# Performance work log

Hardware: AMD Instinct MI355X
Metric: run time of the kernel (lower is better)

Reference implementation:

```python
import jax, jax.numpy as jnp
import numpy as np

B, D, O = 16384, 1024, 2048
MU, LAM = 0.9, 0.1


def setup_inputs() -> dict:
    key = jax.random.key(0)
    ks = jax.random.split(key, 16)
    stdv = float(1.0 / np.sqrt(D))
    u = lambda k, shape, s: jax.random.uniform(k, shape, jnp.float32, -s, s)
    return {
        "x": jax.random.normal(ks[0], (B, D), jnp.float32),
        "x_ctx": jax.random.normal(ks[1], (B, D), jnp.float32),
        "classifier": u(ks[2], (O, D), stdv),
        "none_tensor": u(ks[3], (1, D), stdv),
        "ctx_q_w": u(ks[4], (O, D), stdv),
        "ctx_q_b": u(ks[5], (O,), stdv),
        "word_g_w": u(ks[6], (1, D), stdv),
        "word_g_b": u(ks[7], (1,), stdv),
        "tcq_w1": u(ks[8], (D, D), stdv),
        "tcq_b1": u(ks[9], (D,), stdv),
        "tcq_w2": u(ks[10], (O, D), stdv),
        "tcq_b2": u(ks[11], (O,), stdv),
        "history_input": 0.1 * jax.random.normal(ks[12], (O - 1, D), jnp.float32),
        "history_count": jax.random.randint(ks[13], (O - 1,), 0, 10),
        "labels": jax.random.randint(ks[14], (B,), 0, O),
    }


def reference(x, x_ctx, classifier, none_tensor, ctx_q_w, ctx_q_b,
              word_g_w, word_g_b, tcq_w1, tcq_b1, tcq_w2, tcq_b2,
              history_input, history_count, labels):
    mu, lam = MU, LAM
    # ---- update_history (torch.no_grad), vectorized over classes via segment_sum ----
    xs = jax.lax.stop_gradient(x)
    sums = jax.ops.segment_sum(xs, labels, num_segments=O)               # [O, D]
    counts = jax.ops.segment_sum(jnp.ones((B,), jnp.float32), labels, num_segments=O)  # [O]
    has = counts[1:] > 0                                                  # classes 1..O-1
    cls_mean = sums[1:] / jnp.maximum(counts[1:], 1.0)[:, None]
    hist = jnp.where(has[:, None], mu * history_input + cls_mean, history_input)
    cnt = history_count + has.astype(history_count.dtype)
    # ---- generate_substitute (mu < 1 branch) ----
    denom = 1.0 - jnp.power(mu, jnp.maximum(cnt, 1).astype(jnp.float32))[:, None]
    v = hist * (1.0 - mu) / denom                                        # [O-1, D]
    r_sub = jnp.concatenate([none_tensor, v], axis=0)                    # [O, D]
    ctx_logits = x_ctx @ ctx_q_w.T + ctx_q_b                              # [B, O]
    att_logits = jax.nn.gelu(x @ tcq_w1.T + tcq_b1, approximate=False) @ tcq_w2.T + tcq_b2  # [B, O]
    # ---- gated combine + bilinear classifier (training=True path: w uses ctx_logits) ----
    g_word = jax.nn.sigmoid(x @ word_g_w.T + word_g_b)                    # [B, 1]
    w = g_word * jax.nn.sigmoid(ctx_logits)                               # [B, O]
    # logits = sum(((1-w)*x[:,None,:] + w*r_sub) * classifier, -1), collapsed algebraically
    logits = (1.0 - w) * (x @ classifier.T) + w * jnp.einsum('od,od->o', r_sub, classifier)[None, :]
    # ---- losses on labels >= 0 (mask-weighted means, jit-safe) ----
    mask = (labels >= 0).astype(jnp.float32)
    n = jnp.maximum(mask.sum(), 1.0)
    lsm = jax.nn.log_softmax(logits, axis=-1)
    nll = -jnp.take_along_axis(lsm, jnp.maximum(labels, 0)[:, None], axis=1)[:, 0]
    ce = (mask * nll).sum() / n
    mse_row = jnp.mean((ctx_logits - att_logits) ** 2, axis=-1)
    mse = (mask * mse_row).sum() / n
    return (ce + lam * mse, logits)
```

## Files before the change

### kernel.cpp

```cpp
#include <hip/hip_runtime.h>
#include <cstdint>
#include <cstddef>

#define DEV __device__ __forceinline__

typedef __attribute__((ext_vector_type(4))) float f32x4;
typedef __attribute__((ext_vector_type(8))) short bf16x8;
typedef unsigned short ushort_t;
typedef __attribute__((ext_vector_type(8))) unsigned short ushort8;

static constexpr int B_ = 16384, D_ = 1024, O_ = 2048;
static constexpr float LAM_ = 0.1f;

static constexpr size_t WS_XBF   = 0;
static constexpr size_t WS_XCBF  = WS_XBF   + (size_t)B_ * D_ * 2;
static constexpr size_t WS_HBF   = WS_XCBF  + (size_t)B_ * D_ * 2;
static constexpr size_t WS_CLSBF = WS_HBF   + (size_t)B_ * D_ * 2;
static constexpr size_t WS_CTWBF = WS_CLSBF + (size_t)O_ * D_ * 2;
static constexpr size_t WS_W2BF  = WS_CTWBF + (size_t)O_ * D_ * 2;
static constexpr size_t WS_W1BF  = WS_W2BF  + (size_t)O_ * D_ * 2;
static constexpr size_t WS_SMALL = WS_W1BF  + (size_t)D_ * D_ * 2;
static constexpr size_t SM_COUNTS = 0;
static constexpr size_t SM_TSUM   = 8192;
static constexpr size_t SM_MSE    = 16384;
static constexpr size_t SM_ZERO_BYTES = 82176;
static constexpr size_t SM_S      = 82176;
static constexpr size_t SM_GWORD  = 90368;
static constexpr size_t SM_CEROW  = 155904;

DEV float wave_sum(float v) {
  #pragma unroll
  for (int o = 32; o; o >>= 1) v += __shfl_xor(v, o, 64);
  return v;
}

DEV ushort_t f2bf1(float f) {
  union { float f; unsigned u; } c{f};
  unsigned r = c.u + 0x7fffu + ((c.u >> 16) & 1u);
  return (ushort_t)(r >> 16);
}

DEV float sigmoidf(float z) { return 1.0f / (1.0f + expf(-z)); }

DEV void gload_lds16(const ushort_t* g, ushort_t* l) {
  __builtin_amdgcn_global_load_lds((const __attribute__((address_space(1))) void*)g,
                                   (__attribute__((address_space(3))) void*)l, 16, 0, 0);
}

DEV f32x4 mfma16(bf16x8 a, bf16x8 b, f32x4 c) {
  return __builtin_amdgcn_mfma_f32_16x16x32_bf16(a, b, c, 0, 0, 0);
}

#define DSR(dst, addr, off) \
  asm volatile("ds_read_b128 %0, %1 offset:" off : "=v"(dst) : "v"(addr))

__global__ __launch_bounds__(256) void f2bf_kernel(const float* __restrict__ in,
                                                   ushort_t* __restrict__ out, int n8) {
  int i = blockIdx.x * 256 + threadIdx.x;
  if (i >= n8) return;
  const float4* p = (const float4*)(in + (size_t)i * 8);
  float4 a = p[0], b = p[1];
  ushort8 o;
  o[0] = f2bf1(a.x); o[1] = f2bf1(a.y); o[2] = f2bf1(a.z); o[3] = f2bf1(a.w);
  o[4] = f2bf1(b.x); o[5] = f2bf1(b.y); o[6] = f2bf1(b.z); o[7] = f2bf1(b.w);
  *(ushort8*)(out + (size_t)i * 8) = o;
}

__global__ __launch_bounds__(256) void rowdot_kernel(const float* __restrict__ x,
    const float* __restrict__ cls, const float* __restrict__ wg,
    const float* __restrict__ wgb, const int* __restrict__ labels,
    float* __restrict__ tsum, float* __restrict__ counts, float* __restrict__ g_word) {
  int wave = threadIdx.x >> 6, lane = threadIdx.x & 63;
  int row = blockIdx.x * 4 + wave;
  const float* xr = x + (size_t)row * D_;
  int lab = labels[row];
  const float* cr = cls + (size_t)max(lab, 0) * D_;
  float t = 0.f, g = 0.f;
  #pragma unroll
  for (int j = 0; j < 4; ++j) {
    int d = j * 256 + lane * 4;
    float4 xv = *(const float4*)(xr + d);
    float4 cv = *(const float4*)(cr + d);
    float4 wv = *(const float4*)(wg + d);
    t += xv.x * cv.x + xv.y * cv.y + xv.z * cv.z + xv.w * cv.w;
    g += xv.x * wv.x + xv.y * wv.y + xv.z * wv.z + xv.w * wv.w;
  }
  t = wave_sum(t); g = wave_sum(g);
  if (lane == 0) {
    if (lab >= 0) {
      atomicAdd(&tsum[lab], t);
      atomicAdd(&counts[lab], 1.0f);
    }
    g_word[row] = sigmoidf(g + wgb[0]);
  }
}

__global__ __launch_bounds__(256) void scls_kernel(const float* __restrict__ cls,
    const float* __restrict__ none_t, const float* __restrict__ hist,
    const int* __restrict__ hcnt, const float* __restrict__ counts,
    const float* __restrict__ tsum, float* __restrict__ s) {
  int wave = threadIdx.x >> 6, lane = threadIdx.x & 63;
  int o = blockIdx.x * 4 + wave;
  if (o >= O_) return;
  const float* cr = cls + (size_t)o * D_;
  const float* src = (o == 0) ? none_t : hist + (size_t)(o - 1) * D_;
  float dv = 0.f;
  #pragma unroll
  for (int j = 0; j < 4; ++j) {
    int d = j * 256 + lane * 4;
    float4 a = *(const float4*)(src + d);
    float4 c = *(const float4*)(cr + d);
    dv += a.x * c.x + a.y * c.y + a.z * c.z + a.w * c.w;
  }
  dv = wave_sum(dv);
  if (lane == 0) {
    if (o == 0) { s[0] = dv; }
    else {
      float co = counts[o];
      bool has = co > 0.f;
      int cnt = hcnt[o - 1] + (has ? 1 : 0);
      float denom = 1.f - powf(0.9f, (float)max(cnt, 1));
      float val = has ? (0.9f * dv + tsum[o] / fmaxf(co, 1.f)) : dv;
      s[o] = (0.1f / denom) * val;
    }
  }
}

template<int EPI, int NBN>
__global__ __launch_bounds__(512, 4) void gemm8_kernel(
    const ushort_t* __restrict__ A, const ushort_t* __restrict__ Bmat,
    const float* __restrict__ bias, float* __restrict__ fout,
    ushort_t* __restrict__ hout, const float* __restrict__ g_word,
    const float* __restrict__ svec, float* __restrict__ mse_row) {
  __shared__ __align__(16) ushort_t lds[36864];
  const int tid = threadIdx.x, lane = tid & 63, wave = tid >> 6;
  const int wr = wave >> 1, wc = wave & 1;
  const int nwg = 64 * NBN, cpx = nwg >> 3;
  int bid = blockIdx.x;
  int wg = (bid & 7) * cpx + (bid >> 3);
  const int bm = wg / NBN, bn = wg % NBN;
  const int NCOL = NBN * 128;
  const int qsrc = (tid & 3) ^ ((tid >> 3) & 3);
  const ushort_t* sA0 = A + ((size_t)bm * 256 + (tid >> 2)) * 1024 + qsrc * 8;
  const ushort_t* sB0 = Bmat + ((size_t)bn * 128 + (tid >> 2)) * 1024 + qsrc * 8;
  const int qrd = (lane >> 4) ^ (((lane & 15) >> 1) & 3);
  const unsigned aoffB = (unsigned)(((wr * 64 + (lane & 15)) * 32 + qrd * 8) * 2);
  const unsigned boffB = (unsigned)(((wc * 64 + (lane & 15)) * 32 + qrd * 8) * 2) + 49152u;
  f32x4 acc[4][4] = {};
  gload_lds16(sA0, lds + tid * 8);
  gload_lds16(sA0 + 128 * 1024, lds + (tid + 512) * 8);
  gload_lds16(sB0, lds + 24576 + tid * 8);
  gload_lds16(sA0 + 32, lds + 8192 + tid * 8);
  gload_lds16(sA0 + 32 + 128 * 1024, lds + 8192 + (tid + 512) * 8);
  gload_lds16(sB0 + 32, lds + 24576 + 4096 + tid * 8);
  asm volatile("s_waitcnt vmcnt(3)" ::: "memory");
  __builtin_amdgcn_s_barrier();
  #pragma unroll
  for (int t = 0; t < 32; ++t) {
    const unsigned aA = aoffB + (unsigned)((t % 3) * 16384);
    const unsigned aB = boffB + (unsigned)((t % 3) * 8192);
    bf16x8 fA[4], fB[4];
    DSR(fB[0], aB, "0"); DSR(fB[1], aB, "1024");
    DSR(fB[2], aB, "2048"); DSR(fB[3], aB, "3072");
    DSR(fA[0], aA, "0"); DSR(fA[1], aA, "1024");
    DSR(fA[2], aA, "2048"); DSR(fA[3], aA, "3072");
    if (t < 30) {
      const ushort_t* srcA = sA0 + (size_t)(t + 2) * 32;
      const ushort_t* srcB = sB0 + (size_t)(t + 2) * 32;
      ushort_t* dA = lds + ((t + 2) % 3) * 8192;
      ushort_t* dB = lds + 24576 + ((t + 2) % 3) * 4096;
      gload_lds16(srcA, dA + tid * 8);
      gload_lds16(srcA + 128 * 1024, dA + (tid + 512) * 8);
      gload_lds16(srcB, dB + tid * 8);
    }
    __builtin_amdgcn_s_barrier();
    asm volatile("s_waitcnt lgkmcnt(0)");
    __builtin_amdgcn_sched_barrier(0);
    __builtin_amdgcn_s_setprio(1);
    #pragma unroll
    for (int m = 0; m < 4; m++)
      #pragma unroll
      for (int n = 0; n < 4; n++) acc[m][n] = mfma16(fA[m], fB[n], acc[m][n]);
    __builtin_amdgcn_s_setprio(0);
    __builtin_amdgcn_sched_barrier(0);
    if (t < 30)      asm volatile("s_waitcnt vmcnt(3)" ::: "memory");
    else if (t == 30) asm volatile("s_waitcnt vmcnt(0)" ::: "memory");
    __builtin_amdgcn_s_barrier();
  }
  #pragma unroll
  for (int m = 0; m < 4; m++) {
    #pragma unroll
    for (int i = 0; i < 4; i++) {
      int row = bm * 256 + wr * 64 + m * 16 + (lane >> 4) * 4 + i;
      float gw = 0.f, msum = 0.f;
      if constexpr (EPI == 3) gw = g_word[row];
      #pragma unroll
      for (int n = 0; n < 4; n++) {
        int col = bn * 128 + wc * 64 + n * 16 + (lane & 15);
        float v = acc[m][n][i];
        if constexpr (EPI == 0) {
          float z = v + bias[col];
          float gl = 0.5f * z * (1.f + erff(z * 0.70710678118f));
          hout[(size_t)row * 1024 + col] = f2bf1(gl);
        } else if constexpr (EPI == 1) {
          fout[(size_t)row * NCOL + col] = v + bias[col];
        } else if constexpr (EPI == 2) {
          float att = v + bias[col];
          float ctx = fout[(size_t)row * NCOL + col];
          float d = ctx - att;
          msum += d * d;
        } else {
          size_t off = (size_t)row * NCOL + col;
          float ctx = fout[off];
          float w = gw * sigmoidf(ctx);
          fout[off] = (1.f - w) * v + w * svec[col];
        }
      }
      if constexpr (EPI == 2) {
        #pragma unroll
        for (int o = 1; o < 16; o <<= 1) msum += __shfl_xor(msum, o, 64);
        if ((lane & 15) == 0) atomicAdd(&mse_row[row], msum);
      }
    }
  }
}

__global__ __launch_bounds__(256) void ce_kernel(const float* __restrict__ logits,
    const int* __restrict__ labels, float* __restrict__ ce_row) {
  int row = blockIdx.x, t = threadIdx.x, lane = t & 63, wave = t >> 6;
  const float* lr = logits + (size_t)row * O_;
  float v[8];
  float m = -INFINITY;
  #pragma unroll
  for (int j = 0; j < 8; j++) { v[j] = lr[t + j * 256]; m = fmaxf(m, v[j]); }
  #pragma unroll
  for (int o = 32; o; o >>= 1) m = fmaxf(m, __shfl_xor(m, o, 64));
  __shared__ float red[8];
  if (lane == 0) red[wave] = m;
  __syncthreads();
  m = fmaxf(fmaxf(red[0], red[1]), fmaxf(red[2], red[3]));
  float se = 0.f;
  #pragma unroll
  for (int j = 0; j < 8; j++) se += expf(v[j] - m);
  se = wave_sum(se);
  if (lane == 0) red[4 + wave] = se;
  __syncthreads();
  if (t == 0) {
    float bs = red[4] + red[5] + red[6] + red[7];
    int lab = labels[row];
    float nll = 0.f;
    if (lab >= 0) nll = -(lr[lab] - m - logf(bs));
    ce_row[row] = nll;
  }
}

__global__ __launch_bounds__(256) void finalize_kernel(const float* __restrict__ ce_row,
    const float* __restrict__ mse_row, const int* __restrict__ labels,
    float* __restrict__ out0) {
  int t = threadIdx.x, lane = t & 63, wave = t >> 6;
  float sn = 0.f, sm = 0.f, sc = 0.f;
  for (int i = t; i < B_; i += 256) {
    if (labels[i] >= 0) { sn += ce_row[i]; sm += mse_row[i]; sc += 1.f; }
  }
  sn = wave_sum(sn); sm = wave_sum(sm); sc = wave_sum(sc);
  __shared__ float r0[4], r1[4], r2[4];
  if (lane == 0) { r0[wave] = sn; r1[wave] = sm; r2[wave] = sc; }
  __syncthreads();
  if (t == 0) {
    float a = r0[0] + r0[1] + r0[2] + r0[3];
    float b = r1[0] + r1[1] + r1[2] + r1[3];
    float c = r2[0] + r2[1] + r2[2] + r2[3];
    out0[0] = (a + LAM_ * (b / (float)O_)) / fmaxf(c, 1.f);
  }
}

extern "C" void kernel_launch(void* const* d_in, const int* in_sizes, int n_in,
                              void* d_out, int out_size, void* d_ws, size_t ws_size,
                              hipStream_t stream) {
  const float* x        = (const float*)d_in[0];
  const float* x_ctx    = (const float*)d_in[1];
  const float* cls      = (const float*)d_in[2];
  const float* none_t   = (const float*)d_in[3];
  const float* ctx_q_w  = (const float*)d_in[4];
  const float* ctx_q_b  = (const float*)d_in[5];
  const float* word_g_w = (const float*)d_in[6];
  const float* word_g_b = (const float*)d_in[7];
  const float* w1       = (const float*)d_in[8];
  const float* b1       = (const float*)d_in[9];
  const float* w2       = (const float*)d_in[10];
  const float* b2       = (const float*)d_in[11];
  const float* hist     = (const float*)d_in[12];
  const int*   hcnt     = (const int*)d_in[13];
  const int*   labels   = (const int*)d_in[14];

  float* out  = (float*)d_out;
  float* out1 = out + 1;
  char* ws = (char*)d_ws;

  ushort_t* xbf   = (ushort_t*)(ws + WS_XBF);
  ushort_t* xcbf  = (ushort_t*)(ws + WS_XCBF);
  ushort_t* hbf   = (ushort_t*)(ws + WS_HBF);
  ushort_t* clsbf = (ushort_t*)(ws + WS_CLSBF);
  ushort_t* ctwbf = (ushort_t*)(ws + WS_CTWBF);
  ushort_t* w2bf  = (ushort_t*)(ws + WS_W2BF);
  ushort_t* w1bf  = (ushort_t*)(ws + WS_W1BF);
  float* counts   = (float*)(ws + WS_SMALL + SM_COUNTS);
  float* tsum     = (float*)(ws + WS_SMALL + SM_TSUM);
  float* mse_row  = (float*)(ws + WS_SMALL + SM_MSE);
  float* s        = (float*)(ws + WS_SMALL + SM_S);
  float* g_word   = (float*)(ws + WS_SMALL + SM_GWORD);
  float* ce_row   = (float*)(ws + WS_SMALL + SM_CEROW);

  hipMemsetAsync(ws + WS_SMALL, 0, SM_ZERO_BYTES, stream);

  f2bf_kernel<<<8192, 256, 0, stream>>>(x, xbf, B_ * D_ / 8);
  f2bf_kernel<<<8192, 256, 0, stream>>>(x_ctx, xcbf, B_ * D_ / 8);
  f2bf_kernel<<<1024, 256, 0, stream>>>(cls, clsbf, O_ * D_ / 8);
  f2bf_kernel<<<1024, 256, 0, stream>>>(ctx_q_w, ctwbf, O_ * D_ / 8);
  f2bf_kernel<<<1024, 256, 0, stream>>>(w2, w2bf, O_ * D_ / 8);
  f2bf_kernel<<<512, 256, 0, stream>>>(w1, w1bf, D_ * D_ / 8);

  rowdot_kernel<<<B_ / 4, 256, 0, stream>>>(x, cls, word_g_w, word_g_b, labels,
                                            tsum, counts, g_word);
  scls_kernel<<<O_ / 4, 256, 0, stream>>>(cls, none_t, hist, hcnt, counts, tsum, s);

  gemm8_kernel<0, 8><<<512, 512, 0, stream>>>(xbf, w1bf, b1, nullptr, hbf,
                                              nullptr, nullptr, nullptr);
  gemm8_kernel<1, 16><<<1024, 512, 0, stream>>>(xcbf, ctwbf, ctx_q_b, out1, nullptr,
                                                nullptr, nullptr, nullptr);
  gemm8_kernel<2, 16><<<1024, 512, 0, stream>>>(hbf, w2bf, b2, out1, nullptr,
                                                nullptr, nullptr, mse_row);
  gemm8_kernel<3, 16><<<1024, 512, 0, stream>>>(xbf, clsbf, nullptr, out1, nullptr,
                                                g_word, s, nullptr);

  ce_kernel<<<B_, 256, 0, stream>>>(out1, labels, ce_row);
  finalize_kernel<<<1, 256, 0, stream>>>(ce_row, mse_row, labels, out);
}
```

Baseline: 478.4 us.

## Replace pipelined 256x128 GEMM with simple 128x128 tiles and bf16 ctx buffer

New measurement: 456.1 us. 4.7% less time.

```diff
diff --git a/kernel.cpp b/kernel.cpp
--- a/kernel.cpp
+++ b/kernel.cpp
@@ -27,6 +27,8 @@
 static constexpr size_t SM_S      = 82176;
 static constexpr size_t SM_GWORD  = 90368;
 static constexpr size_t SM_CEROW  = 155904;
+static constexpr size_t WS_CTXBF  = WS_SMALL + 2 * 1024 * 1024;
+static constexpr size_t WS_NEED_BIG = WS_CTXBF + (size_t)B_ * O_ * 2;
 
 DEV float wave_sum(float v) {
   #pragma unroll
@@ -40,6 +42,11 @@
   return (ushort_t)(r >> 16);
 }
 
+DEV float bf2f(ushort_t u) {
+  union { unsigned u; float f; } c{(unsigned)u << 16};
+  return c.f;
+}
+
 DEV float sigmoidf(float z) { return 1.0f / (1.0f + expf(-z)); }
 
 DEV void gload_lds16(const ushort_t* g, ushort_t* l) {
@@ -47,12 +54,17 @@
                                    (__attribute__((address_space(3))) void*)l, 16, 0, 0);
 }
 
+DEV void stage128s(const ushort_t* __restrict__ src, ushort_t* lds_, int tid) {
+  int c0 = tid, c1 = tid + 256;
+  int q0 = (c0 & 3) ^ ((c0 >> 3) & 3);
+  int q1 = (c1 & 3) ^ ((c1 >> 3) & 3);
+  gload_lds16(src + (size_t)(c0 >> 2) * 1024 + q0 * 8, lds_ + c0 * 8);
+  gload_lds16(src + (size_t)(c1 >> 2) * 1024 + q1 * 8, lds_ + c1 * 8);
+}
+
 DEV f32x4 mfma16(bf16x8 a, bf16x8 b, f32x4 c) {
   return __builtin_amdgcn_mfma_f32_16x16x32_bf16(a, b, c, 0, 0, 0);
 }
-
-#define DSR(dst, addr, off) \
-  asm volatile("ds_read_b128 %0, %1 offset:" off : "=v"(dst) : "v"(addr))
 
 __global__ __launch_bounds__(256) void f2bf_kernel(const float* __restrict__ in,
                                                    ushort_t* __restrict__ out, int n8) {
@@ -66,9 +78,10 @@
   *(ushort8*)(out + (size_t)i * 8) = o;
 }
 
-__global__ __launch_bounds__(256) void rowdot_kernel(const float* __restrict__ x,
+__global__ __launch_bounds__(256) void rowdot_cvt_kernel(const float* __restrict__ x,
     const float* __restrict__ cls, const float* __restrict__ wg,
     const float* __restrict__ wgb, const int* __restrict__ labels,
+    ushort_t* __restrict__ xbf,
     float* __restrict__ tsum, float* __restrict__ counts, float* __restrict__ g_word) {
   int wave = threadIdx.x >> 6, lane = threadIdx.x & 63;
   int row = blockIdx.x * 4 + wave;
@@ -84,6 +97,10 @@
     float4 wv = *(const float4*)(wg + d);
     t += xv.x * cv.x + xv.y * cv.y + xv.z * cv.z + xv.w * cv.w;
     g += xv.x * wv.x + xv.y * wv.y + xv.z * wv.z + xv.w * wv.w;
+    uint2 pk;
+    pk.x = (unsigned)f2bf1(xv.x) | ((unsigned)f2bf1(xv.y) << 16);
+    pk.y = (unsigned)f2bf1(xv.z) | ((unsigned)f2bf1(xv.w) << 16);
+    *(uint2*)(xbf + (size_t)row * D_ + d) = pk;
   }
   t = wave_sum(t); g = wave_sum(g);
   if (lane == 0) {
@@ -126,72 +143,47 @@
   }
 }
 
-template<int EPI, int NBN>
-__global__ __launch_bounds__(512, 4) void gemm8_kernel(
+template<int EPI, int NBN, bool CTXB>
+__global__ __launch_bounds__(256, 3) void gemm128_kernel(
     const ushort_t* __restrict__ A, const ushort_t* __restrict__ Bmat,
     const float* __restrict__ bias, float* __restrict__ fout,
-    ushort_t* __restrict__ hout, const float* __restrict__ g_word,
-    const float* __restrict__ svec, float* __restrict__ mse_row) {
-  __shared__ __align__(16) ushort_t lds[36864];
+    ushort_t* __restrict__ hout, ushort_t* __restrict__ ctxbf,
+    const float* __restrict__ g_word, const float* __restrict__ svec,
+    float* __restrict__ mse_row) {
+  __shared__ __align__(16) ushort_t As[128 * 32], Bs[128 * 32];
   const int tid = threadIdx.x, lane = tid & 63, wave = tid >> 6;
   const int wr = wave >> 1, wc = wave & 1;
-  const int nwg = 64 * NBN, cpx = nwg >> 3;
   int bid = blockIdx.x;
-  int wg = (bid & 7) * cpx + (bid >> 3);
-  const int bm = wg / NBN, bn = wg % NBN;
+  int group = bid / (8 * NBN), within = bid % (8 * NBN);
+  int bm = group * 8 + (within & 7);
+  int bn = within >> 3;
   const int NCOL = NBN * 128;
-  const int qsrc = (tid & 3) ^ ((tid >> 3) & 3);
-  const ushort_t* sA0 = A + ((size_t)bm * 256 + (tid >> 2)) * 1024 + qsrc * 8;
-  const ushort_t* sB0 = Bmat + ((size_t)bn * 128 + (tid >> 2)) * 1024 + qsrc * 8;
-  const int qrd = (lane >> 4) ^ (((lane & 15) >> 1) & 3);
-  const unsigned aoffB = (unsigned)(((wr * 64 + (lane & 15)) * 32 + qrd * 8) * 2);
-  const unsigned boffB = (unsigned)(((wc * 64 + (lane & 15)) * 32 + qrd * 8) * 2) + 49152u;
   f32x4 acc[4][4] = {};
-  gload_lds16(sA0, lds + tid * 8);
-  gload_lds16(sA0 + 128 * 1024, lds + (tid + 512) * 8);
-  gload_lds16(sB0, lds + 24576 + tid * 8);
-  gload_lds16(sA0 + 32, lds + 8192 + tid * 8);
-  gload_lds16(sA0 + 32 + 128 * 1024, lds + 8192 + (tid + 512) * 8);
-  gload_lds16(sB0 + 32, lds + 24576 + 4096 + tid * 8);
-  asm volatile("s_waitcnt vmcnt(3)" ::: "memory");
-  __builtin_amdgcn_s_barrier();
-  #pragma unroll
-  for (int t = 0; t < 32; ++t) {
-    const unsigned aA = aoffB + (unsigned)((t % 3) * 16384);
-    const unsigned aB = boffB + (unsigned)((t % 3) * 8192);
-    bf16x8 fA[4], fB[4];
-    DSR(fB[0], aB, "0"); DSR(fB[1], aB, "1024");
-    DSR(fB[2], aB, "2048"); DSR(fB[3], aB, "3072");
-    DSR(fA[0], aA, "0"); DSR(fA[1], aA, "1024");
-    DSR(fA[2], aA, "2048"); DSR(fA[3], aA, "3072");
-    if (t < 30) {
-      const ushort_t* srcA = sA0 + (size_t)(t + 2) * 32;
-      const ushort_t* srcB = sB0 + (size_t)(t + 2) * 32;
-      ushort_t* dA = lds + ((t + 2) % 3) * 8192;
-      ushort_t* dB = lds + 24576 + ((t + 2) % 3) * 4096;
-      gload_lds16(srcA, dA + tid * 8);
-      gload_lds16(srcA + 128 * 1024, dA + (tid + 512) * 8);
-      gload_lds16(srcB, dB + tid * 8);
-    }
+  const ushort_t* Ap = A + (size_t)bm * 128 * 1024;
+  const ushort_t* Bp = Bmat + (size_t)bn * 128 * 1024;
+  const int r = lane & 15;
+  const int qrd8 = ((lane >> 4) ^ ((r >> 1) & 3)) * 8;
+  for (int k0 = 0; k0 < 1024; k0 += 32) {
+    stage128s(Ap + k0, As, tid);
+    stage128s(Bp + k0, Bs, tid);
+    asm volatile("s_waitcnt vmcnt(0)" ::: "memory");
     __builtin_amdgcn_s_barrier();
-    asm volatile("s_waitcnt lgkmcnt(0)");
-    __builtin_amdgcn_sched_barrier(0);
-    __builtin_amdgcn_s_setprio(1);
+    bf16x8 af[4], bf[4];
+    #pragma unroll
+    for (int m = 0; m < 4; m++) af[m] = *(const bf16x8*)&As[(wr * 64 + m * 16 + r) * 32 + qrd8];
+    #pragma unroll
+    for (int n = 0; n < 4; n++) bf[n] = *(const bf16x8*)&Bs[(wc * 64 + n * 16 + r) * 32 + qrd8];
     #pragma unroll
     for (int m = 0; m < 4; m++)
       #pragma unroll
-      for (int n = 0; n < 4; n++) acc[m][n] = mfma16(fA[m], fB[n], acc[m][n]);
-    __builtin_amdgcn_s_setprio(0);
-    __builtin_amdgcn_sched_barrier(0);
-    if (t < 30)      asm volatile("s_waitcnt vmcnt(3)" ::: "memory");
-    else if (t == 30) asm volatile("s_waitcnt vmcnt(0)" ::: "memory");
+      for (int n = 0; n < 4; n++) acc[m][n] = mfma16(af[m], bf[n], acc[m][n]);
     __builtin_amdgcn_s_barrier();
   }
   #pragma unroll
   for (int m = 0; m < 4; m++) {
     #pragma unroll
     for (int i = 0; i < 4; i++) {
-      int row = bm * 256 + wr * 64 + m * 16 + (lane >> 4) * 4 + i;
+      int row = bm * 128 + wr * 64 + m * 16 + (lane >> 4) * 4 + i;
       float gw = 0.f, msum = 0.f;
       if constexpr (EPI == 3) gw = g_word[row];
       #pragma unroll
@@ -203,15 +195,18 @@
           float gl = 0.5f * z * (1.f + erff(z * 0.70710678118f));
           hout[(size_t)row * 1024 + col] = f2bf1(gl);
         } else if constexpr (EPI == 1) {
-          fout[(size_t)row * NCOL + col] = v + bias[col];
+          float z = v + bias[col];
+          if constexpr (CTXB) ctxbf[(size_t)row * O_ + col] = f2bf1(z);
+          else                fout[(size_t)row * NCOL + col] = z;
         } else if constexpr (EPI == 2) {
           float att = v + bias[col];
-          float ctx = fout[(size_t)row * NCOL + col];
+          float ctx = CTXB ? bf2f(ctxbf[(size_t)row * O_ + col])
+                           : fout[(size_t)row * NCOL + col];
           float d = ctx - att;
           msum += d * d;
         } else {
           size_t off = (size_t)row * NCOL + col;
-          float ctx = fout[off];
+          float ctx = CTXB ? bf2f(ctxbf[(size_t)row * O_ + col]) : fout[off];
           float w = gw * sigmoidf(ctx);
           fout[off] = (1.f - w) * v + w * svec[col];
         }
@@ -310,28 +305,47 @@
   float* s        = (float*)(ws + WS_SMALL + SM_S);
   float* g_word   = (float*)(ws + WS_SMALL + SM_GWORD);
   float* ce_row   = (float*)(ws + WS_SMALL + SM_CEROW);
+  ushort_t* ctxbf = (ushort_t*)(ws + WS_CTXBF);
+  const bool big  = ws_size >= WS_NEED_BIG;
 
   hipMemsetAsync(ws + WS_SMALL, 0, SM_ZERO_BYTES, stream);
 
-  f2bf_kernel<<<8192, 256, 0, stream>>>(x, xbf, B_ * D_ / 8);
+  rowdot_cvt_kernel<<<B_ / 4, 256, 0, stream>>>(x, cls, word_g_w, word_g_b, labels,
+                                                xbf, tsum, counts, g_word);
   f2bf_kernel<<<8192, 256, 0, stream>>>(x_ctx, xcbf, B_ * D_ / 8);
   f2bf_kernel<<<1024, 256, 0, stream>>>(cls, clsbf, O_ * D_ / 8);
   f2bf_kernel<<<1024, 256, 0, stream>>>(ctx_q_w, ctwbf, O_ * D_ / 8);
   f2bf_kernel<<<1024, 256, 0, stream>>>(w2, w2bf, O_ * D_ / 8);
   f2bf_kernel<<<512, 256, 0, stream>>>(w1, w1bf, D_ * D_ / 8);
 
-  rowdot_kernel<<<B_ / 4, 256, 0, stream>>>(x, cls, word_g_w, word_g_b, labels,
-                                            tsum, counts, g_word);
   scls_kernel<<<O_ / 4, 256, 0, stream>>>(cls, none_t, hist, hcnt, counts, tsum, s);
 
-  gemm8_kernel<0, 8><<<512, 512, 0, stream>>>(xbf, w1bf, b1, nullptr, hbf,
-                                              nullptr, nullptr, nullptr);
-  gemm8_kernel<1, 16><<<1024, 512, 0, stream>>>(xcbf, ctwbf, ctx_q_b, out1, nullptr,
-                                                nullptr, nullptr, nullptr);
-  gemm8_kernel<2, 16><<<1024, 512, 0, stream>>>(hbf, w2bf, b2, out1, nullptr,
-                                                nullptr, nullptr, mse_row);
-  gemm8_kernel<3, 16><<<1024, 512, 0, stream>>>(xbf, clsbf, nullptr, out1, nullptr,
-                                                g_word, s, nullptr);
+  gemm128_kernel<0, 8, false><<<1024, 256, 0, stream>>>(xbf, w1bf, b1, nullptr, hbf,
+                                                        nullptr, nullptr, nullptr, nullptr);
+  if (big)
+    gemm128_kernel<1, 16, true><<<2048, 256, 0, stream>>>(xcbf, ctwbf, ctx_q_b, out1,
+                                                          nullptr, ctxbf, nullptr, nullptr,
+                                                          nullptr);
+  else
+    gemm128_kernel<1, 16, false><<<2048, 256, 0, stream>>>(xcbf, ctwbf, ctx_q_b, out1,
+                                                           nullptr, nullptr, nullptr, nullptr,
+                                                           nullptr);
+  if (big)
+    gemm128_kernel<2, 16, true><<<2048, 256, 0, stream>>>(hbf, w2bf, b2, out1,
+                                                          nullptr, ctxbf, nullptr, nullptr,
+                                                          mse_row);
+  else
+    gemm128_kernel<2, 16, false><<<2048, 256, 0, stream>>>(hbf, w2bf, b2, out1,
+                                                           nullptr, nullptr, nullptr, nullptr,
+                                                           mse_row);
+  if (big)
+    gemm128_kernel<3, 16, true><<<2048, 256, 0, stream>>>(xbf, clsbf, nullptr, out1,
+                                                          nullptr, ctxbf, g_word, s,
+                                                          nullptr);
+  else
+    gemm128_kernel<3, 16, false><<<2048, 256, 0, stream>>>(xbf, clsbf, nullptr, out1,
+                                                           nullptr, nullptr, g_word, s,
+                                                           nullptr);
 
   ce_kernel<<<B_, 256, 0, stream>>>(out1, labels, ce_row);
   finalize_kernel<<<1, 256, 0, stream>>>(ce_row, mse_row, labels, out);
```
